# Performance work log

Hardware: AMD Instinct MI355X
Metric: run time of the kernel (lower is better)

## Reference

```python
import jax, jax.numpy as jnp
import numpy as np

REG1 = 0.05
REG2 = 0.05

N, D, P = 262144, 256, 512


def setup_inputs() -> dict:
    key = jax.random.key(0)
    kz, kp = jax.random.split(key)
    z = jax.random.normal(kz, (N, D), dtype=jnp.float32)
    # nn.Parameter(torch.rand(P, D)) -> uniform [0, 1)
    prototype_vectors = jax.random.uniform(kp, (P, D), dtype=jnp.float32)
    return {"z": z, "prototype_vectors": prototype_vectors}


def _cdist(a, b):
    # Euclidean pairwise distances [Na, Nb] via the norm trick (matches torch.cdist p=2).
    a2 = jnp.sum(a * a, axis=-1, keepdims=True)          # [Na, 1]
    b2 = jnp.sum(b * b, axis=-1)[None, :]                # [1, Nb]
    sq = a2 + b2 - 2.0 * (a @ b.T)
    return jnp.sqrt(jnp.maximum(sq, 0.0))


def reference(z, prototype_vectors):
    p_dist = _cdist(z, prototype_vectors)                # [N, P]
    f_dist = _cdist(prototype_vectors, z)                # [P, N]
    return (REG1 * jnp.mean(jnp.min(p_dist, axis=1))
            + REG2 * jnp.mean(jnp.min(f_dist, axis=1)))
```

## Files before the change

### kernel.cpp

```cpp
#include <hip/hip_runtime.h>
#include <hip/hip_bf16.h>

#define N_ROWS 262144
#define DDIM   256
#define PROTO  512
#define BM     64
#define RTG    4096
#define NBLK   8192
#define A_STRIDE 264

typedef __bf16 bf16x8 __attribute__((ext_vector_type(8)));
typedef float  f32x4  __attribute__((ext_vector_type(4)));

__global__ void prep_proto(const float* __restrict__ Pm,
                           unsigned short* __restrict__ PBf,
                           float* __restrict__ P2) {
  int p = blockIdx.x;
  int k = threadIdx.x;
  float v = Pm[p * DDIM + k];
  int idx = (p >> 4) * 4096 + (k >> 5) * 512 + ((((k >> 3) & 3) * 16) + (p & 15)) * 8 + (k & 7);
  ((__bf16*)PBf)[idx] = (__bf16)v;
  float sq = v * v;
  #pragma unroll
  for (int m = 1; m < 64; m <<= 1) sq += __shfl_xor(sq, m);
  __shared__ float ws4[4];
  if ((k & 63) == 0) ws4[k >> 6] = sq;
  __syncthreads();
  if (k == 0) P2[p] = (ws4[0] + ws4[1]) + (ws4[2] + ws4[3]);
}

__global__ __launch_bounds__(256, 4)
void proto_main(const float* __restrict__ Z, const unsigned short* __restrict__ PBf,
                const float* __restrict__ P2, float* __restrict__ colpart,
                float* __restrict__ rowminpart) {
  __shared__ __align__(16) unsigned short A_lds[BM * A_STRIDE];
  __shared__ float z2s[BM];
  __shared__ float rowred[BM * 4];

  const int t   = threadIdx.x;
  const int w   = t >> 6;
  const int l   = t & 63;
  const int l15 = l & 15;
  const int lg  = l >> 4;

  const int bid = blockIdx.x;
  const int g   = ((bid >> 4) << 3) | (bid & 7);
  const int cc  = (bid >> 3) & 1;
  const size_t row0 = (size_t)g * BM;

  const int srow = t >> 2;
  const int sc4  = t & 3;
  {
    const float4* Zv = (const float4*)Z + (row0 + srow) * (DDIM / 4);
    float zacc = 0.f;
    #pragma unroll
    for (int m = 0; m < 8; ++m) {
      float4 a0 = Zv[(sc4 + m * 4) * 2];
      float4 a1 = Zv[(sc4 + m * 4) * 2 + 1];
      zacc += a0.x*a0.x + a0.y*a0.y + a0.z*a0.z + a0.w*a0.w
            + a1.x*a1.x + a1.y*a1.y + a1.z*a1.z + a1.w*a1.w;
      bf16x8 pk;
      pk[0] = (__bf16)a0.x; pk[1] = (__bf16)a0.y; pk[2] = (__bf16)a0.z; pk[3] = (__bf16)a0.w;
      pk[4] = (__bf16)a1.x; pk[5] = (__bf16)a1.y; pk[6] = (__bf16)a1.z; pk[7] = (__bf16)a1.w;
      *(bf16x8*)&A_lds[srow * A_STRIDE + (sc4 + m * 4) * 8] = pk;
    }
    zacc += __shfl_xor(zacc, 1);
    zacc += __shfl_xor(zacc, 2);
    if (sc4 == 0) z2s[srow] = zacc;
  }

  float p2r[4];
  #pragma unroll
  for (int j = 0; j < 4; ++j) p2r[j] = P2[cc * 256 + w * 64 + j * 16 + l15];

  __syncthreads();

  f32x4 acc[4][4];
  #pragma unroll
  for (int i = 0; i < 4; ++i)
    #pragma unroll
    for (int j = 0; j < 4; ++j)
      acc[i][j] = (f32x4){0.f, 0.f, 0.f, 0.f};

  const unsigned short* PBw = PBf + (size_t)(cc * 16 + w * 4) * 8 * 512 + l * 8;
  #pragma unroll
  for (int ks = 0; ks < 8; ++ks) {
    bf16x8 af[4];
    #pragma unroll
    for (int i = 0; i < 4; ++i)
      af[i] = *(const bf16x8*)&A_lds[(i * 16 + l15) * A_STRIDE + ks * 32 + lg * 8];
    bf16x8 bg[4];
    #pragma unroll
    for (int j = 0; j < 4; ++j)
      bg[j] = *(const bf16x8*)&PBw[(size_t)(j * 8 + ks) * 512];
    __builtin_amdgcn_s_setprio(1);
    #pragma unroll
    for (int i = 0; i < 4; ++i)
      #pragma unroll
      for (int j = 0; j < 4; ++j)
        acc[i][j] = __builtin_amdgcn_mfma_f32_16x16x32_bf16(af[i], bg[j], acc[i][j], 0, 0, 0);
    __builtin_amdgcn_s_setprio(0);
  }

  float cmin[4] = {3.4e38f, 3.4e38f, 3.4e38f, 3.4e38f};
  #pragma unroll
  for (int i = 0; i < 4; ++i) {
    #pragma unroll
    for (int r = 0; r < 4; ++r) {
      int arow = i * 16 + lg * 4 + r;
      float z2 = z2s[arow];
      float m = 3.4e38f;
      #pragma unroll
      for (int j = 0; j < 4; ++j) {
        float sq = fmaxf(z2 + p2r[j] - 2.0f * acc[i][j][r], 0.0f);
        m = fminf(m, sq);
        cmin[j] = fminf(cmin[j], sq);
      }
      m = fminf(m, __shfl_xor(m, 1));
      m = fminf(m, __shfl_xor(m, 2));
      m = fminf(m, __shfl_xor(m, 4));
      m = fminf(m, __shfl_xor(m, 8));
      if (l15 == 0) rowred[arow * 4 + w] = m;
    }
  }
  #pragma unroll
  for (int j = 0; j < 4; ++j) {
    float c = cmin[j];
    c = fminf(c, __shfl_xor(c, 16));
    c = fminf(c, __shfl_xor(c, 32));
    cmin[j] = c;
  }
  if (l < 16) {
    #pragma unroll
    for (int j = 0; j < 4; ++j)
      colpart[(size_t)g * PROTO + cc * 256 + w * 64 + j * 16 + l] = cmin[j];
  }
  __syncthreads();
  if (t < 64) {
    float m = fminf(fminf(rowred[t * 4], rowred[t * 4 + 1]),
                    fminf(rowred[t * 4 + 2], rowred[t * 4 + 3]));
    rowminpart[(size_t)cc * N_ROWS + row0 + t] = m;
  }
}

__global__ void col_reduce(const float* __restrict__ colpart, float* __restrict__ colfin) {
  int t    = threadIdx.x;
  int colb = blockIdx.x * 16;
  int cl   = t & 15;
  int gg   = t >> 4;
  float m = 3.4e38f;
  for (int g = gg; g < RTG; g += 32)
    m = fminf(m, colpart[(size_t)g * PROTO + colb + cl]);
  m = fminf(m, __shfl_xor(m, 16));
  m = fminf(m, __shfl_xor(m, 32));
  __shared__ float red[8][16];
  if ((t & 63) < 16) red[t >> 6][cl] = m;
  __syncthreads();
  if (t < 16) {
    float r = red[0][t];
    #pragma unroll
    for (int wv = 1; wv < 8; ++wv) r = fminf(r, red[wv][t]);
    colfin[colb + t] = sqrtf(r);
  }
}

__global__ void row_reduce(const float* __restrict__ rowminpart, float* __restrict__ rowsum) {
  int t = threadIdx.x;
  size_t grow = (size_t)blockIdx.x * 256 + t;
  float m = fminf(rowminpart[grow], rowminpart[N_ROWS + grow]);
  float s = sqrtf(m);
  #pragma unroll
  for (int mm = 1; mm < 64; mm <<= 1) s += __shfl_xor(s, mm);
  __shared__ float ws4[4];
  if ((t & 63) == 0) ws4[t >> 6] = s;
  __syncthreads();
  if (t == 0) rowsum[blockIdx.x] = (ws4[0] + ws4[1]) + (ws4[2] + ws4[3]);
}

__global__ void final_reduce(const float* __restrict__ colfin,
                             const float* __restrict__ rowsum,
                             float* __restrict__ out) {
  int t = threadIdx.x;
  float sc = colfin[t];
  float sr = rowsum[t] + rowsum[t + 512];
  #pragma unroll
  for (int mm = 1; mm < 64; mm <<= 1) { sc += __shfl_xor(sc, mm); sr += __shfl_xor(sr, mm); }
  __shared__ float wc[8], wr[8];
  if ((t & 63) == 0) { wc[t >> 6] = sc; wr[t >> 6] = sr; }
  __syncthreads();
  if (t == 0) {
    float tc = 0.f, tr = 0.f;
    #pragma unroll
    for (int i = 0; i < 8; ++i) { tc += wc[i]; tr += wr[i]; }
    out[0] = 0.05f * (tr / (float)N_ROWS) + 0.05f * (tc / (float)PROTO);
  }
}

extern "C" void kernel_launch(void* const* d_in, const int* in_sizes, int n_in,
                              void* d_out, int out_size, void* d_ws, size_t ws_size,
                              hipStream_t stream) {
  const float* z  = (const float*)d_in[0];
  const float* pv = (const float*)d_in[1];
  char* ws = (char*)d_ws;
  size_t off = 0;
  unsigned short* PBf = (unsigned short*)(ws + off); off += 262144;
  float* P2           = (float*)(ws + off);          off += 2048;
  float* colpart      = (float*)(ws + off);          off += (size_t)RTG * PROTO * 4;
  float* colfin       = (float*)(ws + off);          off += 2048;
  float* rowminpart   = (float*)(ws + off);          off += (size_t)2 * N_ROWS * 4;
  float* rowsum       = (float*)(ws + off);          off += 4096;

  prep_proto<<<PROTO, DDIM, 0, stream>>>(pv, PBf, P2);
  proto_main<<<NBLK, 256, 0, stream>>>(z, PBf, P2, colpart, rowminpart);
  col_reduce<<<32, 512, 0, stream>>>(colpart, colfin);
  row_reduce<<<N_ROWS / 256, 256, 0, stream>>>(rowminpart, rowsum);
  final_reduce<<<1, PROTO, 0, stream>>>(colfin, rowsum, (float*)d_out);
}
```

Measured before the change: 145.7 us.

## Process both prototype halves per block to load Z once and fuse row reduction

Each block now loops over both 256-prototype halves, reusing the bf16 Z tile in LDS instead of two blocks each loading and converting the same rows. The row min, sqrt and partial sum are done in-kernel, which removes the row_reduce kernel and its intermediate buffer. The aim is to halve Z global reads and the conversion work. The trade-off is half as many blocks with longer per-block serial work, and the setprio hints are dropped.

```diff
diff --git a/kernel.cpp b/kernel.cpp
--- a/kernel.cpp
+++ b/kernel.cpp
@@ -6,7 +6,6 @@
 #define PROTO  512
 #define BM     64
 #define RTG    4096
-#define NBLK   8192
 #define A_STRIDE 264
 
 typedef __bf16 bf16x8 __attribute__((ext_vector_type(8)));
@@ -32,7 +31,7 @@
 __global__ __launch_bounds__(256, 4)
 void proto_main(const float* __restrict__ Z, const unsigned short* __restrict__ PBf,
                 const float* __restrict__ P2, float* __restrict__ colpart,
-                float* __restrict__ rowminpart) {
+                float* __restrict__ rowsumB) {
   __shared__ __align__(16) unsigned short A_lds[BM * A_STRIDE];
   __shared__ float z2s[BM];
   __shared__ float rowred[BM * 4];
@@ -43,9 +42,7 @@
   const int l15 = l & 15;
   const int lg  = l >> 4;
 
-  const int bid = blockIdx.x;
-  const int g   = ((bid >> 4) << 3) | (bid & 7);
-  const int cc  = (bid >> 3) & 1;
+  const int g = blockIdx.x;
   const size_t row0 = (size_t)g * BM;
 
   const int srow = t >> 2;
@@ -68,78 +65,84 @@
     zacc += __shfl_xor(zacc, 2);
     if (sc4 == 0) z2s[srow] = zacc;
   }
-
-  float p2r[4];
-  #pragma unroll
-  for (int j = 0; j < 4; ++j) p2r[j] = P2[cc * 256 + w * 64 + j * 16 + l15];
-
-  __syncthreads();
-
-  f32x4 acc[4][4];
-  #pragma unroll
-  for (int i = 0; i < 4; ++i)
-    #pragma unroll
-    for (int j = 0; j < 4; ++j)
-      acc[i][j] = (f32x4){0.f, 0.f, 0.f, 0.f};
-
-  const unsigned short* PBw = PBf + (size_t)(cc * 16 + w * 4) * 8 * 512 + l * 8;
-  #pragma unroll
-  for (int ks = 0; ks < 8; ++ks) {
-    bf16x8 af[4];
+  __syncthreads();
+
+  for (int cc = 0; cc < 2; ++cc) {
+    float p2r[4];
+    #pragma unroll
+    for (int j = 0; j < 4; ++j) p2r[j] = P2[cc * 256 + w * 64 + j * 16 + l15];
+
+    f32x4 acc[4][4];
     #pragma unroll
     for (int i = 0; i < 4; ++i)
-      af[i] = *(const bf16x8*)&A_lds[(i * 16 + l15) * A_STRIDE + ks * 32 + lg * 8];
-    bf16x8 bg[4];
-    #pragma unroll
-    for (int j = 0; j < 4; ++j)
-      bg[j] = *(const bf16x8*)&PBw[(size_t)(j * 8 + ks) * 512];
-    __builtin_amdgcn_s_setprio(1);
-    #pragma unroll
-    for (int i = 0; i < 4; ++i)
       #pragma unroll
       for (int j = 0; j < 4; ++j)
-        acc[i][j] = __builtin_amdgcn_mfma_f32_16x16x32_bf16(af[i], bg[j], acc[i][j], 0, 0, 0);
-    __builtin_amdgcn_s_setprio(0);
-  }
-
-  float cmin[4] = {3.4e38f, 3.4e38f, 3.4e38f, 3.4e38f};
-  #pragma unroll
-  for (int i = 0; i < 4; ++i) {
-    #pragma unroll
-    for (int r = 0; r < 4; ++r) {
-      int arow = i * 16 + lg * 4 + r;
-      float z2 = z2s[arow];
-      float m = 3.4e38f;
-      #pragma unroll
-      for (int j = 0; j < 4; ++j) {
-        float sq = fmaxf(z2 + p2r[j] - 2.0f * acc[i][j][r], 0.0f);
-        m = fminf(m, sq);
-        cmin[j] = fminf(cmin[j], sq);
+        acc[i][j] = (f32x4){0.f, 0.f, 0.f, 0.f};
+
+    const unsigned short* PBw = PBf + (size_t)(cc * 16 + w * 4) * 8 * 512 + l * 8;
+    #pragma unroll
+    for (int ks = 0; ks < 8; ++ks) {
+      bf16x8 af[4];
+      #pragma unroll
+      for (int i = 0; i < 4; ++i)
+        af[i] = *(const bf16x8*)&A_lds[(i * 16 + l15) * A_STRIDE + ks * 32 + lg * 8];
+      bf16x8 bg[4];
+      #pragma unroll
+      for (int j = 0; j < 4; ++j)
+        bg[j] = *(const bf16x8*)&PBw[(size_t)(j * 8 + ks) * 512];
+      #pragma unroll
+      for (int i = 0; i < 4; ++i)
+        #pragma unroll
+        for (int j = 0; j < 4; ++j)
+          acc[i][j] = __builtin_amdgcn_mfma_f32_16x16x32_bf16(af[i], bg[j], acc[i][j], 0, 0, 0);
+    }
+
+    float cmin[4] = {3.4e38f, 3.4e38f, 3.4e38f, 3.4e38f};
+    #pragma unroll
+    for (int i = 0; i < 4; ++i) {
+      #pragma unroll
+      for (int r = 0; r < 4; ++r) {
+        int arow = i * 16 + lg * 4 + r;
+        float z2 = z2s[arow];
+        float m = 3.4e38f;
+        #pragma unroll
+        for (int j = 0; j < 4; ++j) {
+          float sq = fmaxf(z2 + p2r[j] - 2.0f * acc[i][j][r], 0.0f);
+          m = fminf(m, sq);
+          cmin[j] = fminf(cmin[j], sq);
+        }
+        m = fminf(m, __shfl_xor(m, 1));
+        m = fminf(m, __shfl_xor(m, 2));
+        m = fminf(m, __shfl_xor(m, 4));
+        m = fminf(m, __shfl_xor(m, 8));
+        if (l15 == 0) {
+          int s = arow * 4 + w;
+          rowred[s] = (cc == 0) ? m : fminf(rowred[s], m);
+        }
       }
-      m = fminf(m, __shfl_xor(m, 1));
-      m = fminf(m, __shfl_xor(m, 2));
-      m = fminf(m, __shfl_xor(m, 4));
-      m = fminf(m, __shfl_xor(m, 8));
-      if (l15 == 0) rowred[arow * 4 + w] = m;
-    }
-  }
-  #pragma unroll
-  for (int j = 0; j < 4; ++j) {
-    float c = cmin[j];
-    c = fminf(c, __shfl_xor(c, 16));
-    c = fminf(c, __shfl_xor(c, 32));
-    cmin[j] = c;
-  }
-  if (l < 16) {
-    #pragma unroll
-    for (int j = 0; j < 4; ++j)
-      colpart[(size_t)g * PROTO + cc * 256 + w * 64 + j * 16 + l] = cmin[j];
-  }
+    }
+    #pragma unroll
+    for (int j = 0; j < 4; ++j) {
+      float c = cmin[j];
+      c = fminf(c, __shfl_xor(c, 16));
+      c = fminf(c, __shfl_xor(c, 32));
+      cmin[j] = c;
+    }
+    if (l < 16) {
+      #pragma unroll
+      for (int j = 0; j < 4; ++j)
+        colpart[(size_t)g * PROTO + cc * 256 + w * 64 + j * 16 + l] = cmin[j];
+    }
+  }
+
   __syncthreads();
   if (t < 64) {
     float m = fminf(fminf(rowred[t * 4], rowred[t * 4 + 1]),
                     fminf(rowred[t * 4 + 2], rowred[t * 4 + 3]));
-    rowminpart[(size_t)cc * N_ROWS + row0 + t] = m;
+    float s = sqrtf(m);
+    s += __shfl_xor(s, 1);  s += __shfl_xor(s, 2);  s += __shfl_xor(s, 4);
+    s += __shfl_xor(s, 8);  s += __shfl_xor(s, 16); s += __shfl_xor(s, 32);
+    if (t == 0) rowsumB[g] = s;
   }
 }
 
@@ -164,25 +167,14 @@
   }
 }
 
-__global__ void row_reduce(const float* __restrict__ rowminpart, float* __restrict__ rowsum) {
-  int t = threadIdx.x;
-  size_t grow = (size_t)blockIdx.x * 256 + t;
-  float m = fminf(rowminpart[grow], rowminpart[N_ROWS + grow]);
-  float s = sqrtf(m);
-  #pragma unroll
-  for (int mm = 1; mm < 64; mm <<= 1) s += __shfl_xor(s, mm);
-  __shared__ float ws4[4];
-  if ((t & 63) == 0) ws4[t >> 6] = s;
-  __syncthreads();
-  if (t == 0) rowsum[blockIdx.x] = (ws4[0] + ws4[1]) + (ws4[2] + ws4[3]);
-}
-
 __global__ void final_reduce(const float* __restrict__ colfin,
-                             const float* __restrict__ rowsum,
+                             const float* __restrict__ rowsumB,
                              float* __restrict__ out) {
   int t = threadIdx.x;
   float sc = colfin[t];
-  float sr = rowsum[t] + rowsum[t + 512];
+  float sr = 0.f;
+  #pragma unroll
+  for (int q = 0; q < 8; ++q) sr += rowsumB[q * 512 + t];
   #pragma unroll
   for (int mm = 1; mm < 64; mm <<= 1) { sc += __shfl_xor(sc, mm); sr += __shfl_xor(sr, mm); }
   __shared__ float wc[8], wr[8];
@@ -207,12 +199,10 @@
   float* P2           = (float*)(ws + off);          off += 2048;
   float* colpart      = (float*)(ws + off);          off += (size_t)RTG * PROTO * 4;
   float* colfin       = (float*)(ws + off);          off += 2048;
-  float* rowminpart   = (float*)(ws + off);          off += (size_t)2 * N_ROWS * 4;
-  float* rowsum       = (float*)(ws + off);          off += 4096;
+  float* rowsumB      = (float*)(ws + off);          off += (size_t)RTG * 4;
 
   prep_proto<<<PROTO, DDIM, 0, stream>>>(pv, PBf, P2);
-  proto_main<<<NBLK, 256, 0, stream>>>(z, PBf, P2, colpart, rowminpart);
+  proto_main<<<RTG, 256, 0, stream>>>(z, PBf, P2, colpart, rowsumB);
   col_reduce<<<32, 512, 0, stream>>>(colpart, colfin);
-  row_reduce<<<N_ROWS / 256, 256, 0, stream>>>(rowminpart, rowsum);
-  final_reduce<<<1, PROTO, 0, stream>>>(colfin, rowsum, (float*)d_out);
-}
+  final_reduce<<<1, PROTO, 0, stream>>>(colfin, rowsumB, (float*)d_out);
+}
```

Result: slower. 452.6 us (+210.6%).
